# Kernel optimization log

Hardware: AMD Instinct MI355X
Metric: run time of the kernel (lower is better)

## Reference

```python
import jax, jax.numpy as jnp
import numpy as np

N, D = 8192, 256
NEG_BIG = -9e15


def setup_inputs() -> dict:
    key = jax.random.key(0)
    k1, k2, k3 = jax.random.split(key, 3)
    h = jax.random.normal(k1, (N, D), dtype=jnp.float32)
    adj = jax.random.randint(k2, (N, N), 0, 2, dtype=jnp.int32)
    # xavier_uniform for a of shape (2D, 1): bound = sqrt(6/(2D+1))
    bound = np.sqrt(6.0 / (2 * D + 1)).astype(np.float32)
    a = jax.random.uniform(k3, (2 * D, 1), dtype=jnp.float32, minval=-bound, maxval=bound)
    return {"h": h, "adj": adj, "a": a}


def reference(h, adj, a):
    d = h.shape[1]
    h1 = h @ a[:d]            # [N, 1]
    h2 = h @ a[d:]            # [N, 1]
    e = jax.nn.leaky_relu(h1 + h2.T, negative_slope=0.01)  # [N, N]
    attention = jnp.where(adj > 0, e, NEG_BIG)
    attention = jax.nn.softmax(attention, axis=1)
    # dropout skipped: eval mode (training=False)
    return attention @ h      # [N, D]
```

## Files before the change

kernel.cpp:

```cpp
#include <hip/hip_runtime.h>
#include <hip/hip_bf16.h>

#define NTOT 8192
#define DDIM 256
#define ROWS 32
#define JSPL 2
#define JHALF (NTOT / JSPL)
#define JCHUNK (JHALF / 8)
#define NITER (JCHUNK / 32)
#define NTSTR 131584
#define HTF_ELEMS (16 * NTSTR)

typedef __attribute__((ext_vector_type(8))) short short8;
typedef __attribute__((ext_vector_type(4))) float floatx4;
typedef __attribute__((ext_vector_type(4))) int intx4;

__global__ __launch_bounds__(256) void gat_scores(const float* __restrict__ h,
                                                  const float* __restrict__ a,
                                                  float4* __restrict__ rc,
                                                  float2* __restrict__ etab) {
  int row  = blockIdx.x * 4 + (threadIdx.x >> 6);
  int lane = threadIdx.x & 63;
  const float* hr = h + (size_t)row * DDIM;
  float p1 = 0.f, p2 = 0.f;
#pragma unroll
  for (int k = 0; k < DDIM / 64; ++k) {
    int idx  = lane + 64 * k;
    float hv = hr[idx];
    p1 += hv * a[idx];
    p2 += hv * a[DDIM + idx];
  }
#pragma unroll
  for (int off = 32; off > 0; off >>= 1) {
    p1 += __shfl_down(p1, off, 64);
    p2 += __shfl_down(p2, off, 64);
  }
  if (lane == 0) {
    rc[row]   = make_float4(__expf(p1), __expf(0.01f * p1), 0.f, 0.f);
    etab[row] = make_float2(__expf(p2), __expf(0.01f * p2));
  }
}

__global__ __launch_bounds__(256) void gat_hpack(const float* __restrict__ h,
                                                 ushort* __restrict__ hTf) {
  __shared__ float tile[64][257];
  const int t    = threadIdx.x;
  const int lane = t & 63;
  const int w    = t >> 6;
  const int quad = lane >> 4;
  const int c    = lane & 15;
  const int i0   = blockIdx.x * 64;

#pragma unroll
  for (int it = 0; it < 16; ++it) {
    int r = it * 4 + w;
    float4 v = *(const float4*)(h + (size_t)(i0 + r) * DDIM + lane * 4);
    tile[r][lane * 4 + 0] = v.x; tile[r][lane * 4 + 1] = v.y;
    tile[r][lane * 4 + 2] = v.z; tile[r][lane * 4 + 3] = v.w;
  }
  __syncthreads();

#pragma unroll
  for (int k = 0; k < 4; ++k) {
    const int n = 4 * k + w;
#pragma unroll
    for (int jbl = 0; jbl < 2; ++jbl) {
      short8 vv;
#pragma unroll
      for (int i = 0; i < 8; ++i) {
        float f = tile[jbl * 32 + quad * 8 + i][n * 16 + c];
        __hip_bfloat16 b = __float2bfloat16(f);
        vv[i] = *(short*)&b;
      }
      *(short8*)(hTf + ((size_t)(n * 257 + i0 / 32 + jbl) * 64 + lane) * 8) = vv;
    }
  }
}

__global__ __launch_bounds__(512, 2) void gat_attn(const ushort* __restrict__ hTf,
                                                   const int* __restrict__ adj,
                                                   const float4* __restrict__ rc,
                                                   const float2* __restrict__ etab,
                                                   float* __restrict__ pout,
                                                   float* __restrict__ plp) {
  __shared__ union {
    float lred[8][32];
    float slab[4][ROWS * 128];
  } sh;

  const int t    = threadIdx.x;
  const int lane = t & 63;
  const int w    = t >> 6;
  const int quad = lane >> 4;
  const int c    = lane & 15;
  const int r0   = blockIdx.x * ROWS;
  const int jb   = blockIdx.y;
  const int jbase = jb * JHALF;

  const float4 rc0 = rc[r0 + c];
  const float4 rc1 = rc[r0 + 16 + c];
  const float E10 = rc0.x, E20 = rc0.y;
  const float E11 = rc1.x, E21 = rc1.y;

  const int* ap0 = adj + (size_t)(r0 + c) * NTOT + jbase + (size_t)w * JCHUNK + quad * 8;
  const int* ap1 = ap0 + (size_t)16 * NTOT;
  const float*  etb = (const float*)(etab + (size_t)jbase + (size_t)w * JCHUNK + quad * 8);
  const ushort* hfp = hTf + (size_t)(jbase / 32 + w * (JCHUNK / 32)) * 512 + lane * 8;

  floatx4 acc[2][16];
#pragma unroll
  for (int rt = 0; rt < 2; ++rt)
#pragma unroll
    for (int nt = 0; nt < 16; ++nt) acc[rt][nt] = (floatx4){0.f, 0.f, 0.f, 0.f};

  float lp0 = 0.f, lp1 = 0.f;
  short8 bA[8], bB[8];

  #define LDH(dst, jt, half)                                                   \
    _Pragma("unroll")                                                          \
    for (int q = 0; q < 8; ++q)                                                \
      dst[q] = *(const short8*)(hfp + (size_t)(jt) * 512 +                     \
                                (size_t)((half) * 8 + q) * NTSTR);

  LDH(bA, 0, 0)
  LDH(bB, 0, 1)
  intx4 A0a = __builtin_nontemporal_load((const intx4*)ap0);
  intx4 A0b = __builtin_nontemporal_load((const intx4*)(ap0 + 4));
  intx4 A1a = __builtin_nontemporal_load((const intx4*)ap1);
  intx4 A1b = __builtin_nontemporal_load((const intx4*)(ap1 + 4));
  float4 ea = ((const float4*)etb)[0];
  float4 eb = ((const float4*)etb)[1];
  float4 ec = ((const float4*)etb)[2];
  float4 ed = ((const float4*)etb)[3];

  for (int jt = 0; jt < NITER; ++jt) {
    const int jn = (jt + 1) & (NITER - 1);

    const int am0[8] = {A0a[0], A0a[1], A0a[2], A0a[3], A0b[0], A0b[1], A0b[2], A0b[3]};
    const int am1[8] = {A1a[0], A1a[1], A1a[2], A1a[3], A1b[0], A1b[1], A1b[2], A1b[3]};
    float tp[16] = {ea.x, ea.y, ea.z, ea.w, eb.x, eb.y, eb.z, eb.w,
                    ec.x, ec.y, ec.z, ec.w, ed.x, ed.y, ed.z, ed.w};
    short8 pa0, pa1;
#pragma unroll
    for (int i = 0; i < 8; ++i) {
      const float t1 = tp[2 * i], t2 = tp[2 * i + 1];
      float p0 = (am0[i] > 0) ? fmaxf(E10 * t1, E20 * t2) : 0.f;
      float p1 = (am1[i] > 0) ? fmaxf(E11 * t1, E21 * t2) : 0.f;
      lp0 += p0; lp1 += p1;
      __hip_bfloat16 b0 = __float2bfloat16(p0);
      __hip_bfloat16 b1 = __float2bfloat16(p1);
      pa0[i] = *(short*)&b0;
      pa1[i] = *(short*)&b1;
    }

    {
      const int* n0 = ap0 + (size_t)jn * 32;
      A0a = __builtin_nontemporal_load((const intx4*)n0);
      A0b = __builtin_nontemporal_load((const intx4*)(n0 + 4));
      const int* n1 = ap1 + (size_t)jn * 32;
      A1a = __builtin_nontemporal_load((const intx4*)n1);
      A1b = __builtin_nontemporal_load((const intx4*)(n1 + 4));
      const float* en = etb + (size_t)jn * 64;
      ea = ((const float4*)en)[0];
      eb = ((const float4*)en)[1];
      ec = ((const float4*)en)[2];
      ed = ((const float4*)en)[3];
    }

#pragma unroll
    for (int q = 0; q < 8; ++q) {
      acc[0][q] = __builtin_amdgcn_mfma_f32_16x16x32_bf16(pa0, bA[q], acc[0][q], 0, 0, 0);
      acc[1][q] = __builtin_amdgcn_mfma_f32_16x16x32_bf16(pa1, bA[q], acc[1][q], 0, 0, 0);
    }
    LDH(bA, jn, 0)

#pragma unroll
    for (int q = 0; q < 8; ++q) {
      acc[0][8 + q] = __builtin_amdgcn_mfma_f32_16x16x32_bf16(pa0, bB[q], acc[0][8 + q], 0, 0, 0);
      acc[1][8 + q] = __builtin_amdgcn_mfma_f32_16x16x32_bf16(pa1, bB[q], acc[1][8 + q], 0, 0, 0);
    }
    LDH(bB, jn, 1)
  }
  #undef LDH

  lp0 += __shfl_xor(lp0, 16, 64); lp0 += __shfl_xor(lp0, 32, 64);
  lp1 += __shfl_xor(lp1, 16, 64); lp1 += __shfl_xor(lp1, 32, 64);
  if (quad == 0) { sh.lred[w][c] = lp0; sh.lred[w][16 + c] = lp1; }
  __syncthreads();

  if (w == 0) {
#pragma unroll
    for (int rt = 0; rt < 2; ++rt)
#pragma unroll
      for (int reg = 0; reg < 4; ++reg) {
        int lrow = rt * 16 + quad * 4 + reg;
        float s = 0.f;
#pragma unroll
        for (int wi = 0; wi < 8; ++wi) s += sh.lred[wi][lrow];
        if (c == 0) plp[(size_t)jb * NTOT + r0 + lrow] = s;
      }
  }
  __syncthreads();

  float* pob = pout + (size_t)jb * NTOT * DDIM;
#pragma unroll
  for (int hd = 0; hd < 2; ++hd) {
    if (w >= 4) {
#pragma unroll
      for (int rt = 0; rt < 2; ++rt)
#pragma unroll
        for (int i = 0; i < 8; ++i)
#pragma unroll
          for (int reg = 0; reg < 4; ++reg)
            sh.slab[w - 4][(rt * 16 + quad * 4 + reg) * 128 + i * 16 + c] =
                acc[rt][i + 8 * hd][reg];
    }
    __syncthreads();
    if (w < 4) {
#pragma unroll
      for (int rt = 0; rt < 2; ++rt)
#pragma unroll
        for (int i = 0; i < 8; ++i)
#pragma unroll
          for (int reg = 0; reg < 4; ++reg)
            acc[rt][i + 8 * hd][reg] +=
                sh.slab[w][(rt * 16 + quad * 4 + reg) * 128 + i * 16 + c];
    }
    __syncthreads();
    if (w == 2 || w == 3) {
#pragma unroll
      for (int rt = 0; rt < 2; ++rt)
#pragma unroll
        for (int i = 0; i < 8; ++i)
#pragma unroll
          for (int reg = 0; reg < 4; ++reg)
            sh.slab[w - 2][(rt * 16 + quad * 4 + reg) * 128 + i * 16 + c] =
                acc[rt][i + 8 * hd][reg];
    }
    __syncthreads();
    if (w < 2) {
#pragma unroll
      for (int rt = 0; rt < 2; ++rt)
#pragma unroll
        for (int i = 0; i < 8; ++i)
#pragma unroll
          for (int reg = 0; reg < 4; ++reg)
            acc[rt][i + 8 * hd][reg] +=
                sh.slab[w][(rt * 16 + quad * 4 + reg) * 128 + i * 16 + c];
    }
    __syncthreads();
    if (w == 1) {
#pragma unroll
      for (int rt = 0; rt < 2; ++rt)
#pragma unroll
        for (int i = 0; i < 8; ++i)
#pragma unroll
          for (int reg = 0; reg < 4; ++reg)
            sh.slab[0][(rt * 16 + quad * 4 + reg) * 128 + i * 16 + c] =
                acc[rt][i + 8 * hd][reg];
    }
    __syncthreads();
    if (w == 0) {
#pragma unroll
      for (int rt = 0; rt < 2; ++rt)
#pragma unroll
        for (int i = 0; i < 8; ++i)
#pragma unroll
          for (int reg = 0; reg < 4; ++reg) {
            float v = acc[rt][i + 8 * hd][reg] +
                      sh.slab[0][(rt * 16 + quad * 4 + reg) * 128 + i * 16 + c];
            pob[(size_t)(r0 + rt * 16 + quad * 4 + reg) * DDIM +
                hd * 128 + i * 16 + c] = v;
          }
    }
    __syncthreads();
  }
}

__global__ __launch_bounds__(256) void gat_combine(const float* __restrict__ pout,
                                                   const float* __restrict__ plp,
                                                   float* __restrict__ out) {
  const int idx = blockIdx.x * 256 + threadIdx.x;
  const int row = idx >> 6;
  float4 a = ((const float4*)pout)[idx];
  float4 b = ((const float4*)(pout + (size_t)NTOT * DDIM))[idx];
  float inv = 1.f / (plp[row] + plp[NTOT + row]);
  float4 r;
  r.x = (a.x + b.x) * inv;
  r.y = (a.y + b.y) * inv;
  r.z = (a.z + b.z) * inv;
  r.w = (a.w + b.w) * inv;
  __builtin_nontemporal_store(r.x, &((float*)out)[idx * 4 + 0]);
  __builtin_nontemporal_store(r.y, &((float*)out)[idx * 4 + 1]);
  __builtin_nontemporal_store(r.z, &((float*)out)[idx * 4 + 2]);
  __builtin_nontemporal_store(r.w, &((float*)out)[idx * 4 + 3]);
}

extern "C" void kernel_launch(void* const* d_in, const int* in_sizes, int n_in,
                              void* d_out, int out_size, void* d_ws, size_t ws_size,
                              hipStream_t stream) {
  const float* h   = (const float*)d_in[0];
  const int*   adj = (const int*)d_in[1];
  const float* a   = (const float*)d_in[2];
  float* out = (float*)d_out;

  float4*   rc    = (float4*)d_ws;
  float2*   etab  = (float2*)(rc + NTOT);
  ushort*   hTf   = (ushort*)(etab + NTOT);
  float*    pout  = (float*)(hTf + HTF_ELEMS);
  float*    plp   = pout + (size_t)JSPL * NTOT * DDIM;

  gat_scores<<<NTOT / 4, 256, 0, stream>>>(h, a, rc, etab);
  gat_hpack<<<NTOT / 64, 256, 0, stream>>>(h, hTf);
  gat_attn<<<dim3(NTOT / ROWS, JSPL), 512, 0, stream>>>(hTf, adj, rc, etab, pout, plp);
  gat_combine<<<(NTOT * DDIM / 4) / 256, 256, 0, stream>>>(pout, plp, out);
}
```

Measured before the change: 438.1 us.

## Split attention work across waves by output columns with shared-memory P tiles

The attention kernel stops giving each wave its own j-range with all 256 output columns. Each wave now owns 32 output columns and covers the full j-range. Waves build the probability tile cooperatively in double-buffered LDS and sync once per 64-column batch. This removes the end-of-kernel cross-wave LDS reduction and cuts the accumulators from 32 floatx4 to 4, which allows 4 blocks per CU instead of 2. The cost is a __syncthreads every iteration and smaller MFMA batches per barrier.

```diff
diff --git a/kernel.cpp b/kernel.cpp
--- a/kernel.cpp
+++ b/kernel.cpp
@@ -6,14 +6,20 @@
 #define ROWS 32
 #define JSPL 2
 #define JHALF (NTOT / JSPL)
-#define JCHUNK (JHALF / 8)
-#define NITER (JCHUNK / 32)
+#define NBATCH 64
 #define NTSTR 131584
 #define HTF_ELEMS (16 * NTSTR)
+#define PSTR 40
 
 typedef __attribute__((ext_vector_type(8))) short short8;
+typedef __attribute__((ext_vector_type(4))) short short4v;
 typedef __attribute__((ext_vector_type(4))) float floatx4;
 typedef __attribute__((ext_vector_type(4))) int intx4;
+
+static __device__ __forceinline__ short bfp(float f) {
+  __hip_bfloat16 b = __float2bfloat16(f);
+  return *(short*)&b;
+}
 
 __global__ __launch_bounds__(256) void gat_scores(const float* __restrict__ h,
                                                   const float* __restrict__ a,
@@ -69,24 +75,21 @@
 #pragma unroll
       for (int i = 0; i < 8; ++i) {
         float f = tile[jbl * 32 + quad * 8 + i][n * 16 + c];
-        __hip_bfloat16 b = __float2bfloat16(f);
-        vv[i] = *(short*)&b;
+        vv[i] = bfp(f);
       }
       *(short8*)(hTf + ((size_t)(n * 257 + i0 / 32 + jbl) * 64 + lane) * 8) = vv;
     }
   }
 }
 
-__global__ __launch_bounds__(512, 2) void gat_attn(const ushort* __restrict__ hTf,
+__global__ __launch_bounds__(512, 4) void gat_attn(const ushort* __restrict__ hTf,
                                                    const int* __restrict__ adj,
                                                    const float4* __restrict__ rc,
                                                    const float2* __restrict__ etab,
                                                    float* __restrict__ pout,
                                                    float* __restrict__ plp) {
-  __shared__ union {
-    float lred[8][32];
-    float slab[4][ROWS * 128];
-  } sh;
+  __shared__ __align__(16) ushort Pb[2][2][32 * PSTR];
+  __shared__ float lsum[8][32];
 
   const int t    = threadIdx.x;
   const int lane = t & 63;
@@ -95,186 +98,110 @@
   const int c    = lane & 15;
   const int r0   = blockIdx.x * ROWS;
   const int jb   = blockIdx.y;
-  const int jbase = jb * JHALF;
-
-  const float4 rc0 = rc[r0 + c];
-  const float4 rc1 = rc[r0 + 16 + c];
-  const float E10 = rc0.x, E20 = rc0.y;
-  const float E11 = rc1.x, E21 = rc1.y;
-
-  const int* ap0 = adj + (size_t)(r0 + c) * NTOT + jbase + (size_t)w * JCHUNK + quad * 8;
-  const int* ap1 = ap0 + (size_t)16 * NTOT;
-  const float*  etb = (const float*)(etab + (size_t)jbase + (size_t)w * JCHUNK + quad * 8);
-  const ushort* hfp = hTf + (size_t)(jbase / 32 + w * (JCHUNK / 32)) * 512 + lane * 8;
-
-  floatx4 acc[2][16];
+
+  const int brow  = lane & 31;
+  const int btile = w & 1;
+  const int bjo   = ((w >> 1) * 2 + (lane >> 5)) * 4;
+  const float4 rcv = rc[r0 + brow];
+  const float E1 = rcv.x, E2 = rcv.y;
+
+  const int*   abase = adj + (size_t)(r0 + brow) * NTOT + (size_t)jb * JHALF + btile * 32 + bjo;
+  const float* ebase = (const float*)(etab + (size_t)jb * JHALF + btile * 32 + bjo);
+  const ushort* hbase = hTf + (size_t)(2 * w) * NTSTR + ((size_t)(jb * 128) * 64 + lane) * 8;
+
+  floatx4 acc[2][2];
 #pragma unroll
   for (int rt = 0; rt < 2; ++rt)
 #pragma unroll
-    for (int nt = 0; nt < 16; ++nt) acc[rt][nt] = (floatx4){0.f, 0.f, 0.f, 0.f};
-
-  float lp0 = 0.f, lp1 = 0.f;
-  short8 bA[8], bB[8];
-
-  #define LDH(dst, jt, half)                                                   \
-    _Pragma("unroll")                                                          \
-    for (int q = 0; q < 8; ++q)                                                \
-      dst[q] = *(const short8*)(hfp + (size_t)(jt) * 512 +                     \
-                                (size_t)((half) * 8 + q) * NTSTR);
-
-  LDH(bA, 0, 0)
-  LDH(bB, 0, 1)
-  intx4 A0a = __builtin_nontemporal_load((const intx4*)ap0);
-  intx4 A0b = __builtin_nontemporal_load((const intx4*)(ap0 + 4));
-  intx4 A1a = __builtin_nontemporal_load((const intx4*)ap1);
-  intx4 A1b = __builtin_nontemporal_load((const intx4*)(ap1 + 4));
-  float4 ea = ((const float4*)etb)[0];
-  float4 eb = ((const float4*)etb)[1];
-  float4 ec = ((const float4*)etb)[2];
-  float4 ed = ((const float4*)etb)[3];
-
-  for (int jt = 0; jt < NITER; ++jt) {
-    const int jn = (jt + 1) & (NITER - 1);
-
-    const int am0[8] = {A0a[0], A0a[1], A0a[2], A0a[3], A0b[0], A0b[1], A0b[2], A0b[3]};
-    const int am1[8] = {A1a[0], A1a[1], A1a[2], A1a[3], A1b[0], A1b[1], A1b[2], A1b[3]};
-    float tp[16] = {ea.x, ea.y, ea.z, ea.w, eb.x, eb.y, eb.z, eb.w,
-                    ec.x, ec.y, ec.z, ec.w, ed.x, ed.y, ed.z, ed.w};
-    short8 pa0, pa1;
-#pragma unroll
-    for (int i = 0; i < 8; ++i) {
-      const float t1 = tp[2 * i], t2 = tp[2 * i + 1];
-      float p0 = (am0[i] > 0) ? fmaxf(E10 * t1, E20 * t2) : 0.f;
-      float p1 = (am1[i] > 0) ? fmaxf(E11 * t1, E21 * t2) : 0.f;
-      lp0 += p0; lp1 += p1;
-      __hip_bfloat16 b0 = __float2bfloat16(p0);
-      __hip_bfloat16 b1 = __float2bfloat16(p1);
-      pa0[i] = *(short*)&b0;
-      pa1[i] = *(short*)&b1;
+    for (int nn = 0; nn < 2; ++nn) acc[rt][nn] = (floatx4){0.f, 0.f, 0.f, 0.f};
+
+  float lps = 0.f, lpdead = 0.f;
+  intx4  ajs[2];
+  float4 es[2][2];
+  short8 bD[2][4];
+
+  #define LDAE(S, bp)                                                          \
+    ajs[S]   = __builtin_nontemporal_load((const intx4*)(abase + (bp) * 64));  \
+    es[S][0] = *(const float4*)(ebase + (bp) * 128);                           \
+    es[S][1] = *(const float4*)(ebase + (bp) * 128 + 4);
+
+  #define LDB(S, bp)                                                           \
+    bD[S][0] = *(const short8*)(hbase + (size_t)((bp) * 2 + 0) * 512);         \
+    bD[S][1] = *(const short8*)(hbase + NTSTR + (size_t)((bp) * 2 + 0) * 512); \
+    bD[S][2] = *(const short8*)(hbase + (size_t)((bp) * 2 + 1) * 512);         \
+    bD[S][3] = *(const short8*)(hbase + NTSTR + (size_t)((bp) * 2 + 1) * 512);
+
+  #define BUILD(S, LACC)                                                       \
+    {                                                                          \
+      short4v pk; float p;                                                     \
+      p = (ajs[S][0] > 0) ? fmaxf(E1 * es[S][0].x, E2 * es[S][0].y) : 0.f; LACC += p; pk[0] = bfp(p); \
+      p = (ajs[S][1] > 0) ? fmaxf(E1 * es[S][0].z, E2 * es[S][0].w) : 0.f; LACC += p; pk[1] = bfp(p); \
+      p = (ajs[S][2] > 0) ? fmaxf(E1 * es[S][1].x, E2 * es[S][1].y) : 0.f; LACC += p; pk[2] = bfp(p); \
+      p = (ajs[S][3] > 0) ? fmaxf(E1 * es[S][1].z, E2 * es[S][1].w) : 0.f; LACC += p; pk[3] = bfp(p); \
+      *(short4v*)&Pb[S][btile][brow * PSTR + bjo] = pk;                        \
     }
 
-    {
-      const int* n0 = ap0 + (size_t)jn * 32;
-      A0a = __builtin_nontemporal_load((const intx4*)n0);
-      A0b = __builtin_nontemporal_load((const intx4*)(n0 + 4));
-      const int* n1 = ap1 + (size_t)jn * 32;
-      A1a = __builtin_nontemporal_load((const intx4*)n1);
-      A1b = __builtin_nontemporal_load((const intx4*)(n1 + 4));
-      const float* en = etb + (size_t)jn * 64;
-      ea = ((const float4*)en)[0];
-      eb = ((const float4*)en)[1];
-      ec = ((const float4*)en)[2];
-      ed = ((const float4*)en)[3];
+  LDAE(0, 0)
+  LDAE(1, 1)
+  LDB(0, 0)
+  LDB(1, 1)
+  BUILD(0, lpdead)
+  __syncthreads();
+
+  #define ITER(bt, CUR, NXT)                                                   \
+    {                                                                          \
+      short8 pa00 = *(const short8*)&Pb[CUR][0][c * PSTR + quad * 8];          \
+      short8 pa01 = *(const short8*)&Pb[CUR][0][(16 + c) * PSTR + quad * 8];   \
+      short8 pa10 = *(const short8*)&Pb[CUR][1][c * PSTR + quad * 8];          \
+      short8 pa11 = *(const short8*)&Pb[CUR][1][(16 + c) * PSTR + quad * 8];   \
+      BUILD(NXT, lps)                                                          \
+      {                                                                        \
+        const int bp = ((bt) + 2) & (NBATCH - 1);                              \
+        LDAE(CUR, bp)                                                          \
+      }                                                                        \
+      acc[0][0] = __builtin_amdgcn_mfma_f32_16x16x32_bf16(pa00, bD[CUR][0], acc[0][0], 0, 0, 0); \
+      acc[0][1] = __builtin_amdgcn_mfma_f32_16x16x32_bf16(pa00, bD[CUR][1], acc[0][1], 0, 0, 0); \
+      acc[1][0] = __builtin_amdgcn_mfma_f32_16x16x32_bf16(pa01, bD[CUR][0], acc[1][0], 0, 0, 0); \
+      acc[1][1] = __builtin_amdgcn_mfma_f32_16x16x32_bf16(pa01, bD[CUR][1], acc[1][1], 0, 0, 0); \
+      acc[0][0] = __builtin_amdgcn_mfma_f32_16x16x32_bf16(pa10, bD[CUR][2], acc[0][0], 0, 0, 0); \
+      acc[0][1] = __builtin_amdgcn_mfma_f32_16x16x32_bf16(pa10, bD[CUR][3], acc[0][1], 0, 0, 0); \
+      acc[1][0] = __builtin_amdgcn_mfma_f32_16x16x32_bf16(pa11, bD[CUR][2], acc[1][0], 0, 0, 0); \
+      acc[1][1] = __builtin_amdgcn_mfma_f32_16x16x32_bf16(pa11, bD[CUR][3], acc[1][1], 0, 0, 0); \
+      {                                                                        \
+        const int bp = ((bt) + 2) & (NBATCH - 1);                              \
+        LDB(CUR, bp)                                                           \
+      }                                                                        \
+      __syncthreads();                                                         \
     }
 
-#pragma unroll
-    for (int q = 0; q < 8; ++q) {
-      acc[0][q] = __builtin_amdgcn_mfma_f32_16x16x32_bf16(pa0, bA[q], acc[0][q], 0, 0, 0);
-      acc[1][q] = __builtin_amdgcn_mfma_f32_16x16x32_bf16(pa1, bA[q], acc[1][q], 0, 0, 0);
-    }
-    LDH(bA, jn, 0)
-
-#pragma unroll
-    for (int q = 0; q < 8; ++q) {
-      acc[0][8 + q] = __builtin_amdgcn_mfma_f32_16x16x32_bf16(pa0, bB[q], acc[0][8 + q], 0, 0, 0);
-      acc[1][8 + q] = __builtin_amdgcn_mfma_f32_16x16x32_bf16(pa1, bB[q], acc[1][8 + q], 0, 0, 0);
-    }
-    LDH(bB, jn, 1)
-  }
-  #undef LDH
-
-  lp0 += __shfl_xor(lp0, 16, 64); lp0 += __shfl_xor(lp0, 32, 64);
-  lp1 += __shfl_xor(lp1, 16, 64); lp1 += __shfl_xor(lp1, 32, 64);
-  if (quad == 0) { sh.lred[w][c] = lp0; sh.lred[w][16 + c] = lp1; }
+  for (int tt = 0; tt < NBATCH; tt += 2) {
+    ITER(tt, 0, 1)
+    ITER(tt + 1, 1, 0)
+  }
+  #undef ITER
+  #undef BUILD
+  #undef LDB
+  #undef LDAE
+
+  lps += __shfl_xor(lps, 32, 64);
+  if (lane < 32) lsum[w][lane] = lps;
   __syncthreads();
-
-  if (w == 0) {
-#pragma unroll
-    for (int rt = 0; rt < 2; ++rt)
-#pragma unroll
-      for (int reg = 0; reg < 4; ++reg) {
-        int lrow = rt * 16 + quad * 4 + reg;
-        float s = 0.f;
-#pragma unroll
-        for (int wi = 0; wi < 8; ++wi) s += sh.lred[wi][lrow];
-        if (c == 0) plp[(size_t)jb * NTOT + r0 + lrow] = s;
-      }
-  }
-  __syncthreads();
+  if (w == 0 && lane < 32) {
+    float s = 0.f;
+#pragma unroll
+    for (int wi = 0; wi < 8; ++wi) s += lsum[wi][lane];
+    plp[(size_t)jb * NTOT + r0 + lane] = s;
+  }
 
   float* pob = pout + (size_t)jb * NTOT * DDIM;
 #pragma unroll
-  for (int hd = 0; hd < 2; ++hd) {
-    if (w >= 4) {
-#pragma unroll
-      for (int rt = 0; rt < 2; ++rt)
-#pragma unroll
-        for (int i = 0; i < 8; ++i)
-#pragma unroll
-          for (int reg = 0; reg < 4; ++reg)
-            sh.slab[w - 4][(rt * 16 + quad * 4 + reg) * 128 + i * 16 + c] =
-                acc[rt][i + 8 * hd][reg];
-    }
-    __syncthreads();
-    if (w < 4) {
-#pragma unroll
-      for (int rt = 0; rt < 2; ++rt)
-#pragma unroll
-        for (int i = 0; i < 8; ++i)
-#pragma unroll
-          for (int reg = 0; reg < 4; ++reg)
-            acc[rt][i + 8 * hd][reg] +=
-                sh.slab[w][(rt * 16 + quad * 4 + reg) * 128 + i * 16 + c];
-    }
-    __syncthreads();
-    if (w == 2 || w == 3) {
-#pragma unroll
-      for (int rt = 0; rt < 2; ++rt)
-#pragma unroll
-        for (int i = 0; i < 8; ++i)
-#pragma unroll
-          for (int reg = 0; reg < 4; ++reg)
-            sh.slab[w - 2][(rt * 16 + quad * 4 + reg) * 128 + i * 16 + c] =
-                acc[rt][i + 8 * hd][reg];
-    }
-    __syncthreads();
-    if (w < 2) {
-#pragma unroll
-      for (int rt = 0; rt < 2; ++rt)
-#pragma unroll
-        for (int i = 0; i < 8; ++i)
-#pragma unroll
-          for (int reg = 0; reg < 4; ++reg)
-            acc[rt][i + 8 * hd][reg] +=
-                sh.slab[w][(rt * 16 + quad * 4 + reg) * 128 + i * 16 + c];
-    }
-    __syncthreads();
-    if (w == 1) {
-#pragma unroll
-      for (int rt = 0; rt < 2; ++rt)
-#pragma unroll
-        for (int i = 0; i < 8; ++i)
-#pragma unroll
-          for (int reg = 0; reg < 4; ++reg)
-            sh.slab[0][(rt * 16 + quad * 4 + reg) * 128 + i * 16 + c] =
-                acc[rt][i + 8 * hd][reg];
-    }
-    __syncthreads();
-    if (w == 0) {
-#pragma unroll
-      for (int rt = 0; rt < 2; ++rt)
-#pragma unroll
-        for (int i = 0; i < 8; ++i)
-#pragma unroll
-          for (int reg = 0; reg < 4; ++reg) {
-            float v = acc[rt][i + 8 * hd][reg] +
-                      sh.slab[0][(rt * 16 + quad * 4 + reg) * 128 + i * 16 + c];
-            pob[(size_t)(r0 + rt * 16 + quad * 4 + reg) * DDIM +
-                hd * 128 + i * 16 + c] = v;
-          }
-    }
-    __syncthreads();
-  }
+  for (int rt = 0; rt < 2; ++rt)
+#pragma unroll
+    for (int nn = 0; nn < 2; ++nn)
+#pragma unroll
+      for (int reg = 0; reg < 4; ++reg)
+        pob[(size_t)(r0 + rt * 16 + quad * 4 + reg) * DDIM + w * 32 + nn * 16 + c] =
+            acc[rt][nn][reg];
 }
 
 __global__ __launch_bounds__(256) void gat_combine(const float* __restrict__ pout,
```

Result: slower. 467.0 us (+6.6%).
